# Kernel tuning notes

Hardware: AMD Instinct MI355X
Metric: run time of the kernel (lower is better)

## Reference

```python
import jax, jax.numpy as jnp
import numpy as np

B, N, E = 4, 10000, 160000
D, H, HID, DE = 128, 4, 128, 16
DK = HID // H


def setup_inputs() -> dict:
    key = jax.random.key(0)
    ks = jax.random.split(key, 16)
    w = lambda k, shape: jax.random.normal(k, shape, jnp.float32) * 0.02
    return {
        "x": jax.random.normal(ks[0], (B, N, D), jnp.float32),
        "edge_index": jax.random.randint(ks[1], (2, E), 0, N, dtype=jnp.int32),
        "edge_attr": jax.random.normal(ks[2], (E, DE), jnp.float32),
        "Wq": w(ks[3], (D, HID)), "bq": jnp.zeros((HID,), jnp.float32),
        "Wk": w(ks[4], (D, HID)), "bk": jnp.zeros((HID,), jnp.float32),
        "Wv": w(ks[5], (D, HID)), "bv": jnp.zeros((HID,), jnp.float32),
        "Wf": w(ks[6], (DE, 2 * HID)), "bf": jnp.zeros((2 * HID,), jnp.float32),
        "Wo": w(ks[7], (HID, D)), "bo": jnp.zeros((D,), jnp.float32),
        "ln_g": jnp.ones((D,), jnp.float32), "ln_b": jnp.zeros((D,), jnp.float32),
    }


def reference(x, edge_index, edge_attr, Wq, bq, Wk, bk, Wv, bv, Wf, bf, Wo, bo, ln_g, ln_b):
    src, dst = edge_index[0], edge_index[1]
    # node projections -> [B, N, H, DK]
    Q = (x @ Wq + bq).reshape(B, N, H, DK)
    K = (x @ Wk + bk).reshape(B, N, H, DK)
    V = (x @ Wv + bv).reshape(B, N, H, DK)
    # edge gathers -> [B, E, H, DK]
    q_e, k_e, v_e = Q[:, dst], K[:, src], V[:, src]
    # FiLM modulation of keys (edge-conditioned, shared across batch)
    gamma, beta = jnp.split(edge_attr @ Wf + bf, 2, axis=-1)
    gamma = gamma.reshape(1, E, H, DK)
    beta = beta.reshape(1, E, H, DK)
    k_e = k_e * (1.0 + gamma) + beta
    logits = (q_e * k_e).sum(-1) / np.sqrt(DK).astype(np.float32)  # [B, E, H]

    def seg_softmax(lg):  # lg: [E, H], softmax over edges sharing a dst node
        m = jax.ops.segment_max(lg, dst, num_segments=N)       # [N, H]
        ex = jnp.exp(lg - m[dst])
        s = jax.ops.segment_sum(ex, dst, num_segments=N)        # [N, H]
        return ex / s[dst]

    att = jax.vmap(seg_softmax)(logits)                         # [B, E, H]
    msg = att[..., None] * v_e                                  # [B, E, H, DK]
    agg = jax.vmap(lambda m: jax.ops.segment_sum(m, dst, num_segments=N))(msg)
    y = agg.reshape(B, N, HID) @ Wo + bo                        # [B, N, D]
    h = x + y  # dropout is identity in eval mode
    mu = h.mean(-1, keepdims=True)
    var = ((h - mu) ** 2).mean(-1, keepdims=True)
    return (h - mu) / jnp.sqrt(var + 1e-5) * ln_g + ln_b
```

## Files before the change

### kernel.cpp

```cpp
#include <hip/hip_runtime.h>
#include <hip/hip_bf16.h>

#define B_ 4
#define N_ 10000
#define E_ 160000
#define D_ 128
#define H_ 4
#define HID_ 128
#define DK_ 32
#define DE_ 16
#define PGRID 2048

typedef __attribute__((ext_vector_type(8))) short short8v;
typedef __attribute__((ext_vector_type(4))) short short4v;
typedef __attribute__((ext_vector_type(4))) float f32x4;
typedef __attribute__((ext_vector_type(2))) float f32x2;

__device__ __forceinline__ short bfb(float f) {
  union { float f; unsigned u; } c; c.f = f;
  unsigned u = c.u + 0x7FFFu + ((c.u >> 16) & 1u);
  return (short)(u >> 16);
}

__device__ __forceinline__ unsigned char f2fp8(float f) {
  int r = __builtin_amdgcn_cvt_pk_fp8_f32(f, f, 0, false);
  return (unsigned char)(r & 0xff);
}
__device__ __forceinline__ f32x2 fp8lo(unsigned u) {
  return __builtin_amdgcn_cvt_pk_f32_fp8((int)u, false);
}
__device__ __forceinline__ f32x2 fp8hi(unsigned u) {
  return __builtin_amdgcn_cvt_pk_f32_fp8((int)u, true);
}

__global__ __launch_bounds__(256) void wt_prep(
    const float* __restrict__ Wq, const float* __restrict__ Wk,
    const float* __restrict__ Wv, const float* __restrict__ Wo,
    short* __restrict__ wt) {
  const float* Ws[4] = {Wq, Wk, Wv, Wo};
  const int i = blockIdx.x * 256 + threadIdx.x;
  const int m = i >> 14;
  const int k = (i >> 7) & 127;
  const int n = i & 127;
  wt[(size_t)m * 16384 + n * 128 + k] = bfb(Ws[m][k * 128 + n]);
}

__global__ __launch_bounds__(64) void qkv_mfma(
    const float* __restrict__ x, const short* __restrict__ wt,
    const float* __restrict__ bq, const float* __restrict__ bk,
    const float* __restrict__ bv,
    float* __restrict__ Q, unsigned char* __restrict__ kv8) {
  __shared__ short xs[16][136];
  const int lane = threadIdx.x;
  const int ln15 = lane & 15;
  const int g    = lane >> 4;
  const long rowBase = (long)blockIdx.x * 16;

  for (int i = lane; i < 16 * 32; i += 64) {
    const int r  = i >> 5;
    const int c4 = (i & 31) * 4;
    const float4 v = *(const float4*)(x + (rowBase + r) * 128 + c4);
    short4v sv; sv.x = bfb(v.x); sv.y = bfb(v.y); sv.z = bfb(v.z); sv.w = bfb(v.w);
    *(short4v*)&xs[r][c4] = sv;
  }
  __syncthreads();

  short8v af[4];
#pragma unroll
  for (int kk = 0; kk < 4; ++kk)
    af[kk] = *(const short8v*)&xs[ln15][kk * 32 + g * 8];

  const float* bs[3] = {bq, bk, bv};

  int bbv[4], nnv[4];
#pragma unroll
  for (int r = 0; r < 4; ++r) {
    const long row = rowBase + g * 4 + r;
    bbv[r] = (int)(row / N_);
    nnv[r] = (int)(row - (long)bbv[r] * N_);
  }

#pragma unroll
  for (int m = 0; m < 3; ++m) {
    const short* Wt = wt + (size_t)m * 16384;
    f32x4 acc[8];
#pragma unroll
    for (int cb = 0; cb < 8; ++cb) acc[cb] = (f32x4){0.f, 0.f, 0.f, 0.f};

#pragma unroll
    for (int kk = 0; kk < 4; ++kk) {
#pragma unroll
      for (int cb = 0; cb < 8; ++cb) {
        const short8v bfr =
            *(const short8v*)(Wt + (cb * 16 + ln15) * 128 + kk * 32 + g * 8);
        acc[cb] = __builtin_amdgcn_mfma_f32_16x16x32_bf16(af[kk], bfr, acc[cb], 0, 0, 0);
      }
    }

    const float* bias = bs[m];
#pragma unroll
    for (int cb = 0; cb < 8; ++cb) {
      const int col = cb * 16 + ln15;
      const float bv_ = bias[col];
#pragma unroll
      for (int r = 0; r < 4; ++r) {
        const float val = acc[cb][r] + bv_;
        if (m == 0) {
          const long row = rowBase + g * 4 + r;
          Q[row * 128 + col] = val;
        } else {
          kv8[(((size_t)nnv[r] * 4 + bbv[r]) << 8) + (m - 1) * 128 + col] = f2fp8(val);
        }
      }
    }
  }
}

__global__ __launch_bounds__(256) void csr_hist(const int* __restrict__ ei,
                                                int* __restrict__ cnt) {
  const int e = blockIdx.x * 256 + threadIdx.x;
  if (e < E_) atomicAdd(&cnt[ei[E_ + e]], 1);
}

__global__ __launch_bounds__(1024) void csr_scan(const int* __restrict__ cnt,
                                                 int* __restrict__ rowptr,
                                                 int* __restrict__ fill) {
  __shared__ int part[1024];
  const int t = threadIdx.x;
  int local[10];
  int sum = 0;
#pragma unroll
  for (int i = 0; i < 10; ++i) {
    const int idx = t * 10 + i;
    local[i] = sum;
    sum += (idx < N_) ? cnt[idx] : 0;
  }
  part[t] = sum;
  __syncthreads();
  for (int off = 1; off < 1024; off <<= 1) {
    const int v = (t >= off) ? part[t - off] : 0;
    __syncthreads();
    part[t] += v;
    __syncthreads();
  }
  const int excl = (t == 0) ? 0 : part[t - 1];
#pragma unroll
  for (int i = 0; i < 10; ++i) {
    const int idx = t * 10 + i;
    if (idx <= N_) {
      const int o = excl + local[i];
      rowptr[idx] = o;
      if (idx < N_) fill[idx] = o;
    }
  }
}

__global__ __launch_bounds__(256) void csr_scatter(
    const int* __restrict__ ei, const float* __restrict__ ea,
    int* __restrict__ fill, int* __restrict__ esrc, float* __restrict__ eas) {
  const int e = blockIdx.x * 256 + threadIdx.x;
  if (e < E_) {
    const int dst = ei[E_ + e];
    const int pos = atomicAdd(&fill[dst], 1);
    esrc[pos] = ei[e];
    const float4* s4 = (const float4*)(ea + (size_t)e * 16);
    float4* d4 = (float4*)(eas + (size_t)pos * 16);
    d4[0] = s4[0]; d4[1] = s4[1]; d4[2] = s4[2]; d4[3] = s4[3];
  }
}

__global__ __launch_bounds__(256) void film_prep(
    const float* __restrict__ eas, const float* __restrict__ Wf,
    const float* __restrict__ bf, unsigned char* __restrict__ film8) {
  const int lane = threadIdx.x & 63;
  const int wave = threadIdx.x >> 6;
  const int c0 = lane * 4;

  float4 w[16];
#pragma unroll
  for (int j = 0; j < 16; ++j) w[j] = *(const float4*)(Wf + j * 256 + c0);
  const float4 bias = *(const float4*)(bf + c0);

  for (int i = blockIdx.x * 4 + wave; i < E_; i += PGRID * 4) {
    const float* ep = eas + (size_t)i * 16;
    const float4 a0 = *(const float4*)ep;
    const float4 a1 = *(const float4*)(ep + 4);
    const float4 a2 = *(const float4*)(ep + 8);
    const float4 a3 = *(const float4*)(ep + 12);
    const float ev[16] = {a0.x,a0.y,a0.z,a0.w, a1.x,a1.y,a1.z,a1.w,
                          a2.x,a2.y,a2.z,a2.w, a3.x,a3.y,a3.z,a3.w};
    float ox = bias.x, oy = bias.y, oz = bias.z, ow = bias.w;
#pragma unroll
    for (int j = 0; j < 16; ++j) {
      ox = fmaf(ev[j], w[j].x, ox);
      oy = fmaf(ev[j], w[j].y, oy);
      oz = fmaf(ev[j], w[j].z, oz);
      ow = fmaf(ev[j], w[j].w, ow);
    }
    int r = __builtin_amdgcn_cvt_pk_fp8_f32(ox, oy, 0, false);
    r = __builtin_amdgcn_cvt_pk_fp8_f32(oz, ow, r, true);
    ((int*)(film8 + (size_t)i * 256))[lane] = r;
  }
}

__global__ __launch_bounds__(256) void fused_attn(
    const int* __restrict__ rowptr, const int* __restrict__ esrc,
    const unsigned char* __restrict__ film8, const float* __restrict__ Q,
    const unsigned char* __restrict__ kv8, float* __restrict__ agg) {
  const int wave = threadIdx.x >> 6;
  const int lane = threadIdx.x & 63;
  const int e2 = lane >> 5;
  const int dh = (lane >> 4) & 1;
  const int b  = (lane >> 2) & 3;
  const int h  = lane & 3;
  const int col0 = h * 32 + dh * 16;

  for (int node = blockIdx.x * 4 + wave; node < N_; node += PGRID * 4) {
    const int beg = rowptr[node], end = rowptr[node + 1];

    float q[16];
    {
      const float* qp = Q + ((size_t)b * N_ + node) * 128 + col0;
#pragma unroll
      for (int c = 0; c < 4; ++c) {
        const float4 t = *(const float4*)(qp + c * 4);
        q[c*4+0] = t.x; q[c*4+1] = t.y; q[c*4+2] = t.z; q[c*4+3] = t.w;
      }
    }
    float acc[16];
#pragma unroll
    for (int d = 0; d < 16; ++d) acc[d] = 0.f;
    float se = 0.f;

    for (int i0 = beg; i0 < end; i0 += 2) {
      const int ii = i0 + e2;
      const bool valid = ii < end;
      const int ic = valid ? ii : i0;
      const int src = esrc[ic];
      const unsigned char* kp = kv8 + ((((size_t)src << 2) + b) << 8) + col0;
      const unsigned char* fp = film8 + (size_t)ic * 256 + col0;
      const uint4 kw = *(const uint4*)kp;
      const uint4 vw = *(const uint4*)(kp + 128);
      const uint4 gw = *(const uint4*)fp;
      const uint4 tw = *(const uint4*)(fp + 128);
      const unsigned ks[4] = {kw.x, kw.y, kw.z, kw.w};
      const unsigned vs[4] = {vw.x, vw.y, vw.z, vw.w};
      const unsigned gs[4] = {gw.x, gw.y, gw.z, gw.w};
      const unsigned ts[4] = {tw.x, tw.y, tw.z, tw.w};

      float pacc[4] = {0.f, 0.f, 0.f, 0.f};
#pragma unroll
      for (int w = 0; w < 4; ++w) {
        const f32x2 k0 = fp8lo(ks[w]), k1 = fp8hi(ks[w]);
        const f32x2 g0 = fp8lo(gs[w]), g1 = fp8hi(gs[w]);
        const f32x2 t0 = fp8lo(ts[w]), t1 = fp8hi(ts[w]);
        float km;
        km = k0.x + fmaf(k0.x, g0.x, t0.x); pacc[w] = fmaf(q[4*w+0], km, pacc[w]);
        km = k0.y + fmaf(k0.y, g0.y, t0.y); pacc[w] = fmaf(q[4*w+1], km, pacc[w]);
        km = k1.x + fmaf(k1.x, g1.x, t1.x); pacc[w] = fmaf(q[4*w+2], km, pacc[w]);
        km = k1.y + fmaf(k1.y, g1.y, t1.y); pacc[w] = fmaf(q[4*w+3], km, pacc[w]);
      }
      float pl = (pacc[0] + pacc[1]) + (pacc[2] + pacc[3]);
      pl += __shfl_xor(pl, 16);

      float ex = __expf(pl * 0.17677669529663687f);
      ex = valid ? ex : 0.f;
      se += ex;
#pragma unroll
      for (int w = 0; w < 4; ++w) {
        const f32x2 v0 = fp8lo(vs[w]), v1 = fp8hi(vs[w]);
        acc[4*w+0] = fmaf(ex, v0.x, acc[4*w+0]);
        acc[4*w+1] = fmaf(ex, v0.y, acc[4*w+1]);
        acc[4*w+2] = fmaf(ex, v1.x, acc[4*w+2]);
        acc[4*w+3] = fmaf(ex, v1.y, acc[4*w+3]);
      }
    }

#pragma unroll
    for (int d = 0; d < 16; ++d) acc[d] += __shfl_xor(acc[d], 32);
    se += __shfl_xor(se, 32);

    if (e2 == 0) {
      const float inv = (end > beg) ? 1.f / se : 0.f;
      float* ap = agg + ((size_t)b * N_ + node) * 128 + col0;
#pragma unroll
      for (int c = 0; c < 4; ++c) {
        float4 o;
        o.x = acc[c*4+0] * inv; o.y = acc[c*4+1] * inv;
        o.z = acc[c*4+2] * inv; o.w = acc[c*4+3] * inv;
        *(float4*)(ap + c * 4) = o;
      }
    }
  }
}

__global__ __launch_bounds__(64) void out_ln_mfma(
    const float* __restrict__ agg, const short* __restrict__ wto,
    const float* __restrict__ bo, const float* __restrict__ x,
    const float* __restrict__ lng, const float* __restrict__ lnb,
    float* __restrict__ out) {
  __shared__ short as_[16][136];
  const int lane = threadIdx.x;
  const int ln15 = lane & 15;
  const int g    = lane >> 4;
  const long rowBase = (long)blockIdx.x * 16;

  for (int i = lane; i < 16 * 32; i += 64) {
    const int r  = i >> 5;
    const int c4 = (i & 31) * 4;
    const float4 v = *(const float4*)(agg + (rowBase + r) * 128 + c4);
    short4v sv; sv.x = bfb(v.x); sv.y = bfb(v.y); sv.z = bfb(v.z); sv.w = bfb(v.w);
    *(short4v*)&as_[r][c4] = sv;
  }
  __syncthreads();

  short8v af[4];
#pragma unroll
  for (int kk = 0; kk < 4; ++kk)
    af[kk] = *(const short8v*)&as_[ln15][kk * 32 + g * 8];

  f32x4 acc[8];
#pragma unroll
  for (int cb = 0; cb < 8; ++cb) acc[cb] = (f32x4){0.f, 0.f, 0.f, 0.f};

#pragma unroll
  for (int kk = 0; kk < 4; ++kk) {
#pragma unroll
    for (int cb = 0; cb < 8; ++cb) {
      const short8v bfr =
          *(const short8v*)(wto + (cb * 16 + ln15) * 128 + kk * 32 + g * 8);
      acc[cb] = __builtin_amdgcn_mfma_f32_16x16x32_bf16(af[kk], bfr, acc[cb], 0, 0, 0);
    }
  }

#pragma unroll
  for (int cb = 0; cb < 8; ++cb) {
    const int col = cb * 16 + ln15;
    const float bov = bo[col];
#pragma unroll
    for (int r = 0; r < 4; ++r) {
      const long row = rowBase + g * 4 + r;
      acc[cb][r] += bov + x[row * 128 + col];
    }
  }

  float s1[4], s2[4];
#pragma unroll
  for (int r = 0; r < 4; ++r) {
    s1[r] = 0.f; s2[r] = 0.f;
#pragma unroll
    for (int cb = 0; cb < 8; ++cb) {
      s1[r] += acc[cb][r];
      s2[r] = fmaf(acc[cb][r], acc[cb][r], s2[r]);
    }
  }
#pragma unroll
  for (int m = 1; m < 16; m <<= 1) {
#pragma unroll
    for (int r = 0; r < 4; ++r) {
      s1[r] += __shfl_xor(s1[r], m);
      s2[r] += __shfl_xor(s2[r], m);
    }
  }
  float mu[4], inv[4];
#pragma unroll
  for (int r = 0; r < 4; ++r) {
    mu[r] = s1[r] * (1.f / 128.f);
    const float var = s2[r] * (1.f / 128.f) - mu[r] * mu[r];
    inv[r] = rsqrtf(var + 1e-5f);
  }

#pragma unroll
  for (int cb = 0; cb < 8; ++cb) {
    const int col = cb * 16 + ln15;
    const float gv = lng[col], bv_ = lnb[col];
#pragma unroll
    for (int r = 0; r < 4; ++r) {
      const long row = rowBase + g * 4 + r;
      out[row * 128 + col] = (acc[cb][r] - mu[r]) * inv[r] * gv + bv_;
    }
  }
}

extern "C" void kernel_launch(void* const* d_in, const int* in_sizes, int n_in,
                              void* d_out, int out_size, void* d_ws, size_t ws_size,
                              hipStream_t stream) {
  const float* x   = (const float*)d_in[0];
  const int*   ei  = (const int*)d_in[1];
  const float* ea  = (const float*)d_in[2];
  const float* Wq  = (const float*)d_in[3];
  const float* bq  = (const float*)d_in[4];
  const float* Wk  = (const float*)d_in[5];
  const float* bk  = (const float*)d_in[6];
  const float* Wv  = (const float*)d_in[7];
  const float* bv  = (const float*)d_in[8];
  const float* Wf  = (const float*)d_in[9];
  const float* bf  = (const float*)d_in[10];
  const float* Wo  = (const float*)d_in[11];
  const float* bo  = (const float*)d_in[12];
  const float* lng = (const float*)d_in[13];
  const float* lnb = (const float*)d_in[14];
  float* out = (float*)d_out;

  const size_t NQ = (size_t)B_ * N_ * HID_;

  char* base = (char*)d_ws;
  size_t off = 0;
  float* Q    = (float*)(base + off); off += NQ * 4;
  float* agg  = (float*)(base + off); off += NQ * 4;
  float* eas  = (float*)(base + off); off += (size_t)E_ * 16 * 4;
  unsigned char* kv8 = (unsigned char*)(base + off);
  off += (size_t)B_ * N_ * 256;
  unsigned char* film8 = (unsigned char*)(base + off);
  off += (size_t)E_ * 256;
  short* wt   = (short*)(base + off); off += 4 * 16384 * 2;
  int*  cnt    = (int*)(base + off); off += N_ * 4;
  int*  rowptr = (int*)(base + off); off += (N_ + 1) * 4;
  int*  fill   = (int*)(base + off); off += N_ * 4;
  int*  esrc   = (int*)(base + off); off += E_ * 4;

  hipMemsetAsync(cnt, 0, N_ * sizeof(int), stream);

  wt_prep<<<256, 256, 0, stream>>>(Wq, Wk, Wv, Wo, wt);
  qkv_mfma<<<(B_ * N_) / 16, 64, 0, stream>>>(x, wt, bq, bk, bv, Q, kv8);
  csr_hist<<<(E_ + 255) / 256, 256, 0, stream>>>(ei, cnt);
  csr_scan<<<1, 1024, 0, stream>>>(cnt, rowptr, fill);
  csr_scatter<<<(E_ + 255) / 256, 256, 0, stream>>>(ei, ea, fill, esrc, eas);
  film_prep<<<PGRID, 256, 0, stream>>>(eas, Wf, bf, film8);
  fused_attn<<<PGRID, 256, 0, stream>>>(rowptr, esrc, film8, Q, kv8, agg);
  out_ln_mfma<<<(B_ * N_) / 16, 64, 0, stream>>>(agg, wt + 3 * 16384, bo, x, lng, lnb, out);
}
```

Before: 175.2 us.

## Store Q in bf16 and scatter FiLM output by position instead of permuting edge attrs

Q is now written as bf16 instead of fp32, which halves its write traffic in the projection kernel and its read traffic in the attention kernel. The CSR scatter no longer copies 64-byte edge attribute rows into sorted order. It records each edge's sorted position, and film_prep reads edge_attr in original order and writes its FiLM output to that position. This removes the intermediate eas buffer round trip at the cost of a slightly lower-precision Q.

```diff
diff --git a/kernel.cpp b/kernel.cpp
--- a/kernel.cpp
+++ b/kernel.cpp
@@ -20,6 +20,10 @@
   union { float f; unsigned u; } c; c.f = f;
   unsigned u = c.u + 0x7FFFu + ((c.u >> 16) & 1u);
   return (short)(u >> 16);
+}
+__device__ __forceinline__ float b2f(unsigned short u) {
+  union { unsigned u; float f; } c; c.u = ((unsigned)u) << 16;
+  return c.f;
 }
 
 __device__ __forceinline__ unsigned char f2fp8(float f) {
@@ -49,7 +53,7 @@
     const float* __restrict__ x, const short* __restrict__ wt,
     const float* __restrict__ bq, const float* __restrict__ bk,
     const float* __restrict__ bv,
-    float* __restrict__ Q, unsigned char* __restrict__ kv8) {
+    unsigned short* __restrict__ Qb, unsigned char* __restrict__ kv8) {
   __shared__ short xs[16][136];
   const int lane = threadIdx.x;
   const int ln15 = lane & 15;
@@ -107,7 +111,7 @@
         const float val = acc[cb][r] + bv_;
         if (m == 0) {
           const long row = rowBase + g * 4 + r;
-          Q[row * 128 + col] = val;
+          Qb[row * 128 + col] = (unsigned short)bfb(val);
         } else {
           kv8[(((size_t)nnv[r] * 4 + bbv[r]) << 8) + (m - 1) * 128 + col] = f2fp8(val);
         }
@@ -156,22 +160,21 @@
 }
 
 __global__ __launch_bounds__(256) void csr_scatter(
-    const int* __restrict__ ei, const float* __restrict__ ea,
-    int* __restrict__ fill, int* __restrict__ esrc, float* __restrict__ eas) {
+    const int* __restrict__ ei, int* __restrict__ fill,
+    int* __restrict__ esrc, int* __restrict__ epos) {
   const int e = blockIdx.x * 256 + threadIdx.x;
   if (e < E_) {
     const int dst = ei[E_ + e];
     const int pos = atomicAdd(&fill[dst], 1);
     esrc[pos] = ei[e];
-    const float4* s4 = (const float4*)(ea + (size_t)e * 16);
-    float4* d4 = (float4*)(eas + (size_t)pos * 16);
-    d4[0] = s4[0]; d4[1] = s4[1]; d4[2] = s4[2]; d4[3] = s4[3];
+    epos[e] = pos;
   }
 }
 
 __global__ __launch_bounds__(256) void film_prep(
-    const float* __restrict__ eas, const float* __restrict__ Wf,
-    const float* __restrict__ bf, unsigned char* __restrict__ film8) {
+    const float* __restrict__ ea, const int* __restrict__ epos,
+    const float* __restrict__ Wf, const float* __restrict__ bf,
+    unsigned char* __restrict__ film8) {
   const int lane = threadIdx.x & 63;
   const int wave = threadIdx.x >> 6;
   const int c0 = lane * 4;
@@ -182,7 +185,7 @@
   const float4 bias = *(const float4*)(bf + c0);
 
   for (int i = blockIdx.x * 4 + wave; i < E_; i += PGRID * 4) {
-    const float* ep = eas + (size_t)i * 16;
+    const float* ep = ea + (size_t)i * 16;
     const float4 a0 = *(const float4*)ep;
     const float4 a1 = *(const float4*)(ep + 4);
     const float4 a2 = *(const float4*)(ep + 8);
@@ -199,13 +202,14 @@
     }
     int r = __builtin_amdgcn_cvt_pk_fp8_f32(ox, oy, 0, false);
     r = __builtin_amdgcn_cvt_pk_fp8_f32(oz, ow, r, true);
-    ((int*)(film8 + (size_t)i * 256))[lane] = r;
+    const int pos = epos[i];
+    ((int*)(film8 + (size_t)pos * 256))[lane] = r;
   }
 }
 
 __global__ __launch_bounds__(256) void fused_attn(
     const int* __restrict__ rowptr, const int* __restrict__ esrc,
-    const unsigned char* __restrict__ film8, const float* __restrict__ Q,
+    const unsigned char* __restrict__ film8, const unsigned short* __restrict__ Qb,
     const unsigned char* __restrict__ kv8, float* __restrict__ agg) {
   const int wave = threadIdx.x >> 6;
   const int lane = threadIdx.x & 63;
@@ -220,11 +224,13 @@
 
     float q[16];
     {
-      const float* qp = Q + ((size_t)b * N_ + node) * 128 + col0;
-#pragma unroll
-      for (int c = 0; c < 4; ++c) {
-        const float4 t = *(const float4*)(qp + c * 4);
-        q[c*4+0] = t.x; q[c*4+1] = t.y; q[c*4+2] = t.z; q[c*4+3] = t.w;
+      const unsigned short* qp = Qb + ((size_t)b * N_ + node) * 128 + col0;
+      const short8v t0 = *(const short8v*)qp;
+      const short8v t1 = *(const short8v*)(qp + 8);
+#pragma unroll
+      for (int j = 0; j < 8; ++j) {
+        q[j]     = b2f((unsigned short)t0[j]);
+        q[8 + j] = b2f((unsigned short)t1[j]);
       }
     }
     float acc[16];
@@ -406,9 +412,8 @@
 
   char* base = (char*)d_ws;
   size_t off = 0;
-  float* Q    = (float*)(base + off); off += NQ * 4;
+  unsigned short* Qb = (unsigned short*)(base + off); off += NQ * 2;
   float* agg  = (float*)(base + off); off += NQ * 4;
-  float* eas  = (float*)(base + off); off += (size_t)E_ * 16 * 4;
   unsigned char* kv8 = (unsigned char*)(base + off);
   off += (size_t)B_ * N_ * 256;
   unsigned char* film8 = (unsigned char*)(base + off);
@@ -418,15 +423,16 @@
   int*  rowptr = (int*)(base + off); off += (N_ + 1) * 4;
   int*  fill   = (int*)(base + off); off += N_ * 4;
   int*  esrc   = (int*)(base + off); off += E_ * 4;
+  int*  epos   = (int*)(base + off); off += E_ * 4;
 
   hipMemsetAsync(cnt, 0, N_ * sizeof(int), stream);
 
   wt_prep<<<256, 256, 0, stream>>>(Wq, Wk, Wv, Wo, wt);
-  qkv_mfma<<<(B_ * N_) / 16, 64, 0, stream>>>(x, wt, bq, bk, bv, Q, kv8);
+  qkv_mfma<<<(B_ * N_) / 16, 64, 0, stream>>>(x, wt, bq, bk, bv, Qb, kv8);
   csr_hist<<<(E_ + 255) / 256, 256, 0, stream>>>(ei, cnt);
   csr_scan<<<1, 1024, 0, stream>>>(cnt, rowptr, fill);
-  csr_scatter<<<(E_ + 255) / 256, 256, 0, stream>>>(ei, ea, fill, esrc, eas);
-  film_prep<<<PGRID, 256, 0, stream>>>(eas, Wf, bf, film8);
-  fused_attn<<<PGRID, 256, 0, stream>>>(rowptr, esrc, film8, Q, kv8, agg);
+  csr_scatter<<<(E_ + 255) / 256, 256, 0, stream>>>(ei, fill, esrc, epos);
+  film_prep<<<PGRID, 256, 0, stream>>>(ea, epos, Wf, bf, film8);
+  fused_attn<<<PGRID, 256, 0, stream>>>(rowptr, esrc, film8, Qb, kv8, agg);
   out_ln_mfma<<<(B_ * N_) / 16, 64, 0, stream>>>(agg, wt + 3 * 16384, bo, x, lng, lnb, out);
 }
```

New measurement: 171.2 us. 2.3% less time.
